# Kernel tuning notes

Hardware: AMD Instinct MI355X
Metric: run time of the kernel (lower is better)

Reference implementation:

```python
import jax, jax.numpy as jnp
import numpy as np

B, N, DE, DH, L, DC = 8, 256, 768, 192, 2, 192
NEG = 1e30  # mask_logic constant from the repo


def setup_inputs() -> dict:
    ks = iter(jax.random.split(jax.random.key(0), 32))

    def nrm(shape, s=0.02):
        return jax.random.normal(next(ks), shape, dtype=jnp.float32) * s

    features = jax.random.normal(next(ks), (B, N, DE), dtype=jnp.float32)
    # DAG adjacency: node i attends to a subset of j < i; guarantee edge (i, i-1)
    rnd = jax.random.bernoulli(next(ks), 0.3, (B, N, N))
    tril = jnp.tril(jnp.ones((N, N), jnp.bool_), -1)
    adj = ((rnd & tril[None]) | jnp.eye(N, k=-1, dtype=jnp.bool_)[None]).astype(jnp.float32)
    s_mask = jax.random.bernoulli(next(ks), 0.5, (B, N, N)).astype(jnp.float32)
    s_mask_onehot = jnp.stack([1.0 - s_mask, s_mask], axis=-1)  # unused in forward
    lengths = jnp.full((B,), N, dtype=jnp.int32)  # unused (nodal_att_type=None)
    return dict(
        features=features, adj=adj, s_mask=s_mask,
        s_mask_onehot=s_mask_onehot, lengths=lengths,
        fc1_w=nrm((DE, DH)), fc1_b=jnp.zeros((DH,), jnp.float32),
        gat_w=nrm((L, 2 * DH)), gat_b=jnp.zeros((L,), jnp.float32),
        wr0=nrm((L, DH, DH)), wr1=nrm((L, DH, DH)),
        gruc_wih=nrm((L, 3 * DH, DH)), gruc_whh=nrm((L, 3 * DH, DH)),
        gruc_bih=jnp.zeros((L, 3 * DH), jnp.float32),
        gruc_bhh=jnp.zeros((L, 3 * DH), jnp.float32),
        grup_wih=nrm((L, 3 * DH, DH)), grup_whh=nrm((L, 3 * DH, DH)),
        grup_bih=jnp.zeros((L, 3 * DH), jnp.float32),
        grup_bhh=jnp.zeros((L, 3 * DH), jnp.float32),
        mlp_w0=nrm((DH * (L + 1), DH)), mlp_b0=jnp.zeros((DH,), jnp.float32),
        mlp_w1=nrm((DH, DH)), mlp_b1=jnp.zeros((DH,), jnp.float32),
        mlp_w2=nrm((DH, DC)), mlp_b2=jnp.zeros((DC,), jnp.float32),
    )


def _gru(x, h, wih, whh, bih, bhh):
    # torch.nn.GRUCell math
    gi = x @ wih.T + bih
    gh = h @ whh.T + bhh
    ir, iz, inn = jnp.split(gi, 3, axis=-1)
    hr, hz, hn = jnp.split(gh, 3, axis=-1)
    r = jax.nn.sigmoid(ir + hr)
    z = jax.nn.sigmoid(iz + hz)
    n = jnp.tanh(inn + r * hn)
    return (1.0 - z) * n + z * h


def _layer(Hl, adj, s_mask, gat_w, gat_b, wr0, wr1, cw, cp):
    # One DAG layer: sequential scan over nodes. Carry holds the relation-
    # projected value buffers V0=H1@Wr0^T, V1=H1@Wr1^T and per-node key
    # scores Ksc=H1@wk (rows >= i are zero and masked out), which is
    # mathematically identical to the torch code that re-projects the
    # growing H1 every step.
    wq, wk = gat_w[:DH], gat_w[DH:]
    pos = jnp.arange(N)

    def step(carry, xs):
        V0, V1, Ksc = carry
        i, x_i, adj_i, sm_i = xs  # x_i:(B,DH) adj_i,sm_i:(B,N)
        score = (x_i @ wq)[:, None] + Ksc + gat_b          # (B,N)
        mask = (pos < i)[None, :] & (adj_i > 0.5)          # ragged :i slice
        alpha = jnp.where(mask, score, score - NEG)        # mask_logic
        attn = jax.nn.softmax(alpha, axis=-1)              # masked -> exactly 0
        Vrel = V0 * sm_i[..., None] + V1 * (1.0 - sm_i[..., None])
        M = jnp.einsum('bn,bnd->bd', attn, Vrel)
        M = jnp.where(i > 0, M, 0.0)                       # node 0: no context
        C = _gru(x_i, M, *cw)
        P = _gru(M, x_i, *cp)
        Hnew = C + P
        V0 = V0.at[:, i, :].set(Hnew @ wr0.T)
        V1 = V1.at[:, i, :].set(Hnew @ wr1.T)
        Ksc = Ksc.at[:, i].set(Hnew @ wk)
        attn_out = jnp.where(i > 0, attn, 0.0)             # adjB row 0 is zeros
        return (V0, V1, Ksc), (Hnew, attn_out)

    z3 = jnp.zeros((B, N, DH), jnp.float32)
    carry0 = (z3, z3, jnp.zeros((B, N), jnp.float32))
    xs = (pos, Hl.transpose(1, 0, 2), adj.transpose(1, 0, 2), s_mask.transpose(1, 0, 2))
    _, (Hseq, Aseq) = jax.lax.scan(step, carry0, xs)
    return Hseq.transpose(1, 0, 2), Aseq.transpose(1, 0, 2)  # (B,N,DH),(B,N,N)


def reference(features, adj, s_mask, s_mask_onehot, lengths,
              fc1_w, fc1_b, gat_w, gat_b, wr0, wr1,
              gruc_wih, gruc_whh, gruc_bih, gruc_bhh,
              grup_wih, grup_whh, grup_bih, grup_bhh,
              mlp_w0, mlp_b0, mlp_w1, mlp_b1, mlp_w2, mlp_b2):
    Hl = jax.nn.relu(features @ fc1_w + fc1_b)  # H0
    Hs, As = [Hl], []
    for l in range(L):
        cw = (gruc_wih[l], gruc_whh[l], gruc_bih[l], gruc_bhh[l])
        cp = (grup_wih[l], grup_whh[l], grup_bih[l], grup_bhh[l])
        Hl, Al = _layer(Hl, adj, s_mask, gat_w[l], gat_b[l], wr0[l], wr1[l], cw, cp)
        Hs.append(Hl)
        As.append(Al)
    H = jnp.concatenate(Hs, axis=2)  # (B,N,DH*(L+1))
    # nodal_att_type=None => attentive_node_features is identity
    h = jax.nn.relu(H @ mlp_w0 + mlp_b0)
    h = jax.nn.relu(h @ mlp_w1 + mlp_b1)  # mlp_layers-1 = 1 extra block
    logits = h @ mlp_w2 + mlp_b2          # dropout: eval-mode identity
    return logits, jnp.stack(As, axis=1)  # (B,N,DC), (B,L,N,N)
```

## Files before the change

### kernel.cpp

```cpp
#include <hip/hip_runtime.h>
#include <stdint.h>

#define B_  8
#define N_  256
#define DH_ 192
#define L_  2
#define G3  576
#define G6  1152
#define NW  4
#define DS  48
#define KD  24
#define GC  288
#define MPSZ (8 * NW * DH_ * 3)
#define KDSZ (8 * NW)
#define STH 10001
#define STP 20001
#define STQ 25001
#define SPK 50000
#define SF1 50001
#define SF2 50002
#define SDN 60001

typedef unsigned long long u64;

__device__ __forceinline__ float bflo(uint32_t u) { return __uint_as_float(u << 16); }
__device__ __forceinline__ float bfhi(uint32_t u) { return __uint_as_float(u & 0xffff0000u); }
__device__ __forceinline__ uint32_t f2bf(float f) {
    uint32_t x = __float_as_uint(f);
    x += 0x7fffu + ((x >> 16) & 1u);
    return x >> 16;
}
__device__ __forceinline__ float sigm(float x)  { return 1.f / (1.f + __expf(-x)); }
__device__ __forceinline__ float tanhf_(float x){ return 1.f - 2.f / (1.f + __expf(2.f * x)); }
__device__ __forceinline__ u64 packvs(float v, int st) {
    return ((u64)(uint32_t)st << 32) | __float_as_uint(v);
}
__device__ __forceinline__ u64 agload(const u64* p) {
    return __hip_atomic_load(p, __ATOMIC_RELAXED, __HIP_MEMORY_SCOPE_AGENT);
}
__device__ __forceinline__ void agstore(u64* p, u64 v) {
    __hip_atomic_store(p, v, __ATOMIC_RELAXED, __HIP_MEMORY_SCOPE_AGENT);
}
__device__ __forceinline__ float u2f(u64 v) { return __uint_as_float((uint32_t)v); }

struct ScanSm {
    uint4 Wr4s[12 * DH_];
    float sA0[2][N_], sA1[2][N_], sKsc[N_];
    float sAdjN[N_], sSmN[N_];
    float sXq[2][DH_];
    float sPre[6 * DS], sXv[DS];
    float sM[DH_], su0[DS], su1[DS], sGc[GC], sHn[DS];
    float sRl[DH_], sP0l[DH_], sP1l[DH_];
    float sRedS[2][8], sRedX[3], sSaved[8], sSavedA[2], sSavedS[2];
};
struct WorkSm {
    float sX[DH_];
    float sPv[GC];
    float sRed[3];
};
struct PrologSm {
    float sA[8][768];
    float sRed[3][8][192];
};
struct MlpSm {
    float sH[8][576];
    float sRed[3][8][192];
    float sT[8][192];
};
union SmemAll { ScanSm s; WorkSm w; PrologSm p; MlpSm m; };

__device__ void prepack_slice(int idx,
    const float* __restrict__ wr0, const float* __restrict__ wr1,
    const float* __restrict__ c_wih, const float* __restrict__ c_whh,
    const float* __restrict__ c_bih, const float* __restrict__ c_bhh,
    const float* __restrict__ p_wih, const float* __restrict__ p_whh,
    const float* __restrict__ p_bih, const float* __restrict__ p_bhh,
    float* __restrict__ WpreT, uint32_t* __restrict__ W4,
    uint32_t* __restrict__ Wr4, uint32_t* __restrict__ Wp4w,
    float* __restrict__ biasPre, float* __restrict__ gbx)
{
    for (int l = 0; l < L_; ++l) {
        const float* cwih = c_wih + l * G3 * DH_;
        const float* cwhh = c_whh + l * G3 * DH_;
        const float* pwih = p_wih + l * G3 * DH_;
        const float* pwhh = p_whh + l * G3 * DH_;
        if (l == 0) {
            int k = idx / G6, r = idx - k * G6;
            float w = (r < G3) ? cwih[r * DH_ + k] : pwhh[(r - G3) * DH_ + k];
            WpreT[k * G6 + r] = w;
        }
        if (idx < NW * 27648) {
// ... 101 lines not shown
                const float* b0 = WpreT + t;
                float a0[8] = {0.f,0.f,0.f,0.f,0.f,0.f,0.f,0.f};
                float a1[8] = {0.f,0.f,0.f,0.f,0.f,0.f,0.f,0.f};
                #pragma unroll 4
                for (int k = 0; k < 192; ++k) {
                    float bva = b0[(size_t)k * G6];
                    float bvb = b0[(size_t)k * G6 + 576];
                    #pragma unroll
                    for (int rr = 0; rr < 8; ++rr) {
                        float av = P->sA[rr][k];
                        a0[rr] += av * bva; a1[rr] += av * bvb;
                    }
                }
                #pragma unroll
                for (int rr = 0; rr < 8; ++rr) {
                    PREg[(size_t)(r0 + rr) * G6 + t]       = a0[rr] + bpa;
                    PREg[(size_t)(r0 + rr) * G6 + 576 + t] = a1[rr] + bpb;
                }
            }
            __syncthreads();
        }
    }
    flag_sync(Fp + 192, wgid, t, SF2);
}

__device__ void mlp_tail(char* smem, int wgid, int t,
    const float* __restrict__ Hcat,
    const float* __restrict__ mw0, const float* __restrict__ mb0,
    const float* __restrict__ mw1, const float* __restrict__ mb1,
    const float* __restrict__ mw2, const float* __restrict__ mb2,
    float* __restrict__ out, u64* __restrict__ Fd)
{
    if (t < 64) {
        while ((uint32_t)(agload(&Fd[t]) >> 32) != (uint32_t)SDN) {}
    }
    __syncthreads();
    __threadfence();
    __syncthreads();
    MlpSm* M = (MlpSm*)smem;
    const int c = t % 192, kg = t / 192;
    for (int tt = wgid; tt < 256; tt += 96) {
        const int r0 = tt * 8;
        for (int q = t; q < 1152; q += 576) {
            int r = q / 144, c4 = q % 144;
            *(float4*)&M->sH[r][4 * c4] = *(const float4*)(Hcat + (size_t)(r0 + r) * G3 + 4 * c4);
        }
        __syncthreads();
        {
            const float* bp = mw0 + (size_t)(kg * 192) * 192 + c;
            float acc[8] = {0.f,0.f,0.f,0.f,0.f,0.f,0.f,0.f};
            #pragma unroll 8
            for (int kk = 0; kk < 192; ++kk) {
                float bv = bp[(size_t)kk * 192];
                #pragma unroll
                for (int rr = 0; rr < 8; ++rr) acc[rr] += M->sH[rr][kg * 192 + kk] * bv;
            }
            #pragma unroll
            for (int rr = 0; rr < 8; ++rr) M->sRed[kg][rr][c] = acc[rr];
        }
        __syncthreads();
        if (t < 192) {
            float bv = mb0[t];
            #pragma unroll
            for (int rr = 0; rr < 8; ++rr)
                M->sT[rr][t] = fmaxf(M->sRed[0][rr][t] + M->sRed[1][rr][t] + M->sRed[2][rr][t] + bv, 0.f);
        }
        __syncthreads();
// ... 19 lines not shown
        __syncthreads();
        {
            const float* bp = mw2 + (size_t)(kg * 64) * 192 + c;
            float acc[8] = {0.f,0.f,0.f,0.f,0.f,0.f,0.f,0.f};
            #pragma unroll 8
            for (int kk = 0; kk < 64; ++kk) {
                float bv = bp[(size_t)kk * 192];
                #pragma unroll
                for (int rr = 0; rr < 8; ++rr) acc[rr] += M->sH[rr][kg * 64 + kk] * bv;
            }
            #pragma unroll
            for (int rr = 0; rr < 8; ++rr) M->sRed[kg][rr][c] = acc[rr];
        }
        __syncthreads();
        if (t < 192) {
            float bv = mb2[t];
            #pragma unroll
            for (int rr = 0; rr < 8; ++rr)
                out[(size_t)(r0 + rr) * 192 + t] =
                    M->sRed[0][rr][t] + M->sRed[1][rr][t] + M->sRed[2][rr][t] + bv;
        }
        __syncthreads();
    }
}

template<int ISL2>
__device__ void scan_body(
    ScanSm* S, int b, int w, int t,
    const float* __restrict__ xin, float* __restrict__ hout,
    const float* __restrict__ PREg, const float* __restrict__ adj,
    const float* __restrict__ smask,
    const uint32_t* __restrict__ W4l, const uint32_t* __restrict__ Wr4l,
    const float* __restrict__ gbxl, const float* __restrict__ gatwl,
    uint32_t* __restrict__ Hw, u64* __restrict__ MPsl, u64* __restrict__ Kdl,
    u64* __restrict__ HcW, const u64* __restrict__ HcR,
    const u64* __restrict__ PREcR, const u64* __restrict__ XQcR,
    float* __restrict__ AsB, int sbase)
{
    const int lane = t & 63, wave = t >> 6;
    const int dg0 = w * DS;
    const float* adjB = adj   + (size_t)b * N_ * N_;
    const float* smB  = smask + (size_t)b * N_ * N_;
    const int fi = b * NW;
    const int cB4 = t >> 1, khB4 = t & 1;

    {
        uint32_t* wr = (uint32_t*)S->Wr4s;
        for (int q = t; q < 9216; q += 576) wr[q] = Wr4l[q];
    }
    uint4 wreg[12];
    {
        const uint4* W4v = (const uint4*)W4l;
        #pragma unroll
        for (int p4 = 0; p4 < 12; ++p4) wreg[p4] = W4v[(12 * khB4 + p4) * GC + cB4];
    }
    float wqx = (!ISL2 && t >= 192 && t < 384) ? gatwl[t - 192] : 0.f;
    float wkv = 0.f, g2b = 0.f, g5b = 0.f;
    if (t < DS) { wkv = gatwl[DH_ + dg0 + t]; g2b = gbxl[dg0 + t]; g5b = gbxl[DH_ + dg0 + t]; }
    if (t < N_) { S->sKsc[t] = 0.f; S->sA0[1][t] = 0.f; S->sA1[1][t] = 0.f; }
    if (t < DS) { S->su0[t] = 0.f; S->su1[t] = 0.f; }
    if (t < 5)  S->sRedS[1][t] = 0.f;
    if (w == 0 && t < N_) AsB[t] = 0.f;

    if (!ISL2) {
        if (t < DS) {
            const float* pre = PREg + (size_t)(b * N_) * G6 + dg0 + t;
            S->sPre[t] = pre[0]; S->sPre[DS + t] = pre[192]; S->sPre[2 * DS + t] = pre[384];
            S->sPre[3 * DS + t] = pre[576]; S->sPre[4 * DS + t] = pre[768]; S->sPre[5 * DS + t] = pre[960];
            S->sXv[t] = xin[(size_t)(b * N_) * G3 + dg0 + t];
        }
        for (int q = t; q < 224; q += 576) {
            if (q < 64)       *(float4*)&S->sAdjN[4 * q] = *(const float4*)(adjB + N_ + 4 * q);
            else if (q < 128) { int q2 = q - 64;  *(float4*)&S->sSmN[4 * q2] = *(const float4*)(smB + N_ + 4 * q2); }
            else if (q < 176) { int q2 = q - 128; *(float4*)&S->sXq[1][4 * q2] = *(const float4*)(xin + (size_t)(b * N_ + 1) * G3 + 4 * q2); }
            else              { int q2 = q - 176; *(float4*)&S->sXq[0][4 * q2] = *(const float4*)(xin + (size_t)(b * N_ + 2) * G3 + 4 * q2); }
        }
    } else {
        for (int q = t; q < 321; q += 576) {
            if (q < 64)       *(float4*)&S->sAdjN[4 * q] = *(const float4*)(adjB + N_ + 4 * q);
            else if (q < 128) { int q2 = q - 64;  *(float4*)&S->sSmN[4 * q2] = *(const float4*)(smB + N_ + 4 * q2); }
            else if (q < 176) {
                int d = q - 128;
                const u64* p = HcR + ((size_t)(b * N_) * NW + w) * DS + d;
                u64 v; do { v = agload(p); } while ((uint32_t)(v >> 32) != (uint32_t)STH);
                S->sXv[d] = __uint_as_float((uint32_t)v);
            } else if (q < 320) {
                int qq = q - 176;
                const u64* p = PREcR + ((size_t)(b * N_) * NW + w) * 144 + qq;
                u64 v; do { v = agload(p); } while ((uint32_t)(v >> 32) != (uint32_t)STP);
                uint32_t pl = (uint32_t)v;
                S->sPre[2 * qq] = bflo(pl); S->sPre[2 * qq + 1] = bfhi(pl);
            } else {
                const u64* p = XQcR + b * N_ + 1;
                u64 v; do { v = agload(p); } while ((uint32_t)(v >> 32) != (uint32_t)(STQ + 1));
                S->sSaved[3] = __uint_as_float((uint32_t)v);
            }
        }
    }
    __syncthreads();
    {
        float hn = 0.f;
        if (t < DS) {
            float xv = S->sXv[t];
            float r1 = sigm(S->sPre[t]), z1 = sigm(S->sPre[DS + t]);
            float n1 = tanhf_(S->sPre[2 * DS + t] + r1 * g2b);
            float Cv = (1.f - z1) * n1;
            float r2 = sigm(S->sPre[3 * DS + t]), z2 = sigm(S->sPre[4 * DS + t]);
            float n2 = tanhf_(g5b + r2 * S->sPre[5 * DS + t]);
            hn = Cv + (1.f - z2) * n2 + z2 * xv;
            S->sHn[t] = hn;
            hout[(size_t)(b * N_) * G3 + dg0 + t] = hn;
            if (!ISL2) HcW[((size_t)(b * N_) * NW + w) * DS + t] = packvs(hn, STH);
        }
        if (t == 0) { S->sSavedA[1] = S->sAdjN[0]; S->sSavedS[1] = S->sSmN[0]; }
        if (wave == 0) {
            float v = hn * wkv;
            #pragma unroll
            for (int o = 32; o; o >>= 1) v += __shfl_xor(v, o);
            if (lane == 0) { S->sSaved[6] = v; agstore(&Kdl[fi + w], packvs(v, sbase)); }
        }
    }
    __syncthreads();
    if (t < KD) Hw[(size_t)t * N_] = f2bf(S->sHn[2 * t]) | (f2bf(S->sHn[2 * t + 1]) << 16);
    if (!ISL2 && t >= 192 && t < 384) {
        float px = S->sXq[1][t - 192] * wqx;
        #pragma unroll
        for (int o = 32; o; o >>= 1) px += __shfl_xor(px, o);
        if (lane == 0) S->sRedX[wave - 3] = px;
    }
    __syncthreads();
    float xqc = ISL2 ? S->sSaved[3] : (S->sRedX[0] + S->sRedX[1] + S->sRedX[2]);

    for (int i = 1; i < N_; ++i) {
        const int row = b * N_ + i;
        const int stamp = sbase + i;
        const int pp = i & 1, pn = pp ^ 1;

        if (t < DH_) {
            float rr = 0.f, p0 = 0.f, p1 = 0.f;
            #pragma unroll 4
            for (int kq = 0; kq < 12; ++kq) {
                uint4 wv = S->Wr4s[kq * DH_ + t];
                const int k0 = 4 * kq;
                float lo, hi;
                lo = bflo(wv.x); hi = bfhi(wv.x);
                rr = fmaf(S->su0[k0 + 0], lo, rr); rr = fmaf(S->su1[k0 + 0], hi, rr);
                p0 = fmaf(S->sHn[k0 + 0], lo, p0); p1 = fmaf(S->sHn[k0 + 0], hi, p1);
                lo = bflo(wv.y); hi = bfhi(wv.y);
                rr = fmaf(S->su0[k0 + 1], lo, rr); rr = fmaf(S->su1[k0 + 1], hi, rr);
                p0 = fmaf(S->sHn[k0 + 1], lo, p0); p1 = fmaf(S->sHn[k0 + 1], hi, p1);
                lo = bflo(wv.z); hi = bfhi(wv.z);
                rr = fmaf(S->su0[k0 + 2], lo, rr); rr = fmaf(S->su1[k0 + 2], hi, rr);
                p0 = fmaf(S->sHn[k0 + 2], lo, p0); p1 = fmaf(S->sHn[k0 + 2], hi, p1);
                lo = bflo(wv.w); hi = bfhi(wv.w);
                rr = fmaf(S->su0[k0 + 3], lo, rr); rr = fmaf(S->su1[k0 + 3], hi, rr);
                p0 = fmaf(S->sHn[k0 + 3], lo, p0); p1 = fmaf(S->sHn[k0 + 3], hi, p1);
            }
            S->sRl[t] = rr; S->sP0l[t] = p0; S->sP1l[t] = p1;
            u64* base = &MPsl[(size_t)pp * MPSZ + ((size_t)(fi + w) * DH_ + t) * 3];
            agstore(base + 0, packvs(rr, stamp));
            agstore(base + 1, packvs(p0, stamp));
            agstore(base + 2, packvs(p1, stamp));
        } else if (t < 384) {
            if (!ISL2) {
                float px = S->sXq[(i - 1) & 1][t - 192] * wqx;
                #pragma unroll
                for (int o = 32; o; o >>= 1) px += __shfl_xor(px, o);
                if (lane == 0) S->sRedX[wave - 3] = px;
            }
        } else {
            const int u = t - 384;
            const int inx = (i + 1 < N_) ? i + 1 : N_ - 1;
            if (!ISL2) {
                const int ixq = (i + 2 < N_) ? i + 2 : N_ - 1;
                for (int qq = u; qq < 260; qq += 192) {
                    if (qq < 64)
                        *(float4*)&S->sAdjN[4 * qq] = *(const float4*)(adjB + (size_t)inx * N_ + 4 * qq);
                    else if (qq < 128) { int q2 = qq - 64;
                        *(float4*)&S->sSmN[4 * q2] = *(const float4*)(smB + (size_t)inx * N_ + 4 * q2); }
                    else if (qq < 140) { int q2 = qq - 128;
                        *(float4*)&S->sXv[4 * q2] = *(const float4*)(xin + (size_t)row * G3 + dg0 + 4 * q2); }
                    else if (qq < 212) { int q2 = qq - 140; int g = q2 / 12, o = q2 - 12 * g;
                        *(float4*)&S->sPre[g * DS + 4 * o] =
                            *(const float4*)(PREg + (size_t)row * G6 + g * DH_ + dg0 + 4 * o); }
                    else { int q2 = qq - 212;
                        *(float4*)&S->sXq[i & 1][4 * q2] = *(const float4*)(xin + (size_t)(b * N_ + ixq) * G3 + 4 * q2); }
                }
            } else {
                for (int qq = u; qq < 321; qq += 192) {
                    if (qq < 64)
                        *(float4*)&S->sAdjN[4 * qq] = *(const float4*)(adjB + (size_t)inx * N_ + 4 * qq);
                    else if (qq < 128) { int q2 = qq - 64;
                        *(float4*)&S->sSmN[4 * q2] = *(const float4*)(smB + (size_t)inx * N_ + 4 * q2); }
                    else if (qq < 176) {
                        int d = qq - 128;
                        const u64* p = HcR + ((size_t)row * NW + w) * DS + d;
                        u64 v; do { v = agload(p); } while ((uint32_t)(v >> 32) != (uint32_t)(STH + i));
                        S->sXv[d] = __uint_as_float((uint32_t)v);
                    } else if (qq < 320) {
                        int q2 = qq - 176;
                        const u64* p = PREcR + ((size_t)row * NW + w) * 144 + q2;
                        u64 v; do { v = agload(p); } while ((uint32_t)(v >> 32) != (uint32_t)(STP + i));
                        uint32_t pl = (uint32_t)v;
                        S->sPre[2 * q2] = bflo(pl); S->sPre[2 * q2 + 1] = bfhi(pl);
                    } else {
                        const u64* p = XQcR + b * N_ + inx;
                        u64 v; do { v = agload(p); } while ((uint32_t)(v >> 32) != (uint32_t)(STQ + inx));
                        S->sSaved[3] = __uint_as_float((uint32_t)v);
                    }
                }
            }
        }
        __syncthreads();

        const float xqn = ISL2 ? S->sSaved[3] : (S->sRedX[0] + S->sRedX[1] + S->sRedX[2]);
        if (t < N_) {
            float e = 0.f;
            if (t == i) { S->sSavedA[pn] = S->sAdjN[t]; S->sSavedS[pn] = S->sSmN[t]; }
            if (t < i - 1 && S->sAdjN[t] > 0.5f) e = __expf(xqn + S->sKsc[t]);
            float b0 = e * S->sSmN[t];
            S->sA0[pn][t] = b0; S->sA1[pn][t] = e - b0;
            float ps = e;
            #pragma unroll
            for (int o = 32; o; o >>= 1) ps += __shfl_xor(ps, o);
            if (lane == 0) S->sRedS[pn][wave] = ps;
        }
        __syncthreads();

        if (t < 384) {
            const int ilim = i - 1;
            const int kd = t >> 4, jp = t & 15;
            const uint32_t* hp = Hw + (size_t)kd * N_;
            float u0l = 0.f, u0h = 0.f, u1l = 0.f, u1h = 0.f;
            int j = jp;
            while (j + 48 < ilim) {
                uint32_t h0 = hp[j], h1 = hp[j + 16], h2 = hp[j + 32], h3 = hp[j + 48];
                float b0, b1;
                b0 = S->sA0[pn][j];      b1 = S->sA1[pn][j];
                u0l = fmaf(b0, bflo(h0), u0l); u0h = fmaf(b0, bfhi(h0), u0h);
                u1l = fmaf(b1, bflo(h0), u1l); u1h = fmaf(b1, bfhi(h0), u1h);
                b0 = S->sA0[pn][j + 16]; b1 = S->sA1[pn][j + 16];
                u0l = fmaf(b0, bflo(h1), u0l); u0h = fmaf(b0, bfhi(h1), u0h);
                u1l = fmaf(b1, bflo(h1), u1l); u1h = fmaf(b1, bfhi(h1), u1h);
                b0 = S->sA0[pn][j + 32]; b1 = S->sA1[pn][j + 32];
                u0l = fmaf(b0, bflo(h2), u0l); u0h = fmaf(b0, bfhi(h2), u0h);
                u1l = fmaf(b1, bflo(h2), u1l); u1h = fmaf(b1, bfhi(h2), u1h);
                b0 = S->sA0[pn][j + 48]; b1 = S->sA1[pn][j + 48];
                u0l = fmaf(b0, bflo(h3), u0l); u0h = fmaf(b0, bfhi(h3), u0h);
                u1l = fmaf(b1, bflo(h3), u1l); u1h = fmaf(b1, bfhi(h3), u1h);
                j += 64;
            }
            for (; j < ilim; j += 16) {
                uint32_t hv = hp[j];
                float b0 = S->sA0[pn][j], b1 = S->sA1[pn][j];
                u0l = fmaf(b0, bflo(hv), u0l); u0h = fmaf(b0, bfhi(hv), u0h);
                u1l = fmaf(b1, bflo(hv), u1l); u1h = fmaf(b1, bfhi(hv), u1h);
            }
            #pragma unroll
            for (int o = 1; o <= 8; o <<= 1) {
                u0l += __shfl_xor(u0l, o); u0h += __shfl_xor(u0h, o);
                u1l += __shfl_xor(u1l, o); u1h += __shfl_xor(u1h, o);
            }
            if (jp == 0) {
                S->su0[2 * kd] = u0l; S->su0[2 * kd + 1] = u0h;
                S->su1[2 * kd] = u1l; S->su1[2 * kd + 1] = u1h;
            }
        } else {
            const int d = t - 384;
            const int w1 = (w + 1) & 3, w2 = (w + 2) & 3, w3 = (w + 3) & 3;
            const u64* pA = &MPsl[(size_t)pp * MPSZ + ((size_t)(fi + w1) * DH_ + d) * 3];
            const u64* pB = &MPsl[(size_t)pp * MPSZ + ((size_t)(fi + w2) * DH_ + d) * 3];
            const u64* pC = &MPsl[(size_t)pp * MPSZ + ((size_t)(fi + w3) * DH_ + d) * 3];
            const uint32_t ex = (uint32_t)stamp;
            u64 a0, a1, a2, b0, b1, b2, c0, c1, c2;
            do {
                a0 = agload(pA); a1 = agload(pA + 1); a2 = agload(pA + 2);
                b0 = agload(pB); b1 = agload(pB + 1); b2 = agload(pB + 2);
                c0 = agload(pC); c1 = agload(pC + 1); c2 = agload(pC + 2);
            } while ((uint32_t)(a0 >> 32) != ex || (uint32_t)(a1 >> 32) != ex ||
                     (uint32_t)(a2 >> 32) != ex || (uint32_t)(b0 >> 32) != ex ||
                     (uint32_t)(b1 >> 32) != ex || (uint32_t)(b2 >> 32) != ex ||
                     (uint32_t)(c0 >> 32) != ex || (uint32_t)(c1 >> 32) != ex ||
                     (uint32_t)(c2 >> 32) != ex);
            S->sRl[d]  += u2f(a0) + u2f(b0) + u2f(c0);
            S->sP0l[d] += u2f(a1) + u2f(b1) + u2f(c1);
            S->sP1l[d] += u2f(a2) + u2f(b2) + u2f(c2);
            if (t == 575) {
                const uint32_t ex2 = (uint32_t)(stamp - 1);
                const int kpar = (i - 1) & 1;
                u64 k0, k1, k2;
                u64* q1 = &Kdl[kpar * KDSZ + fi + w1];
                u64* q2 = &Kdl[kpar * KDSZ + fi + w2];
                u64* q3 = &Kdl[kpar * KDSZ + fi + w3];
                do {
                    k0 = agload(q1); k1 = agload(q2); k2 = agload(q3);
                } while ((uint32_t)(k0 >> 32) != ex2 || (uint32_t)(k1 >> 32) != ex2 ||
                         (uint32_t)(k2 >> 32) != ex2);
                float kdot = S->sSaved[6] + u2f(k0) + u2f(k1) + u2f(k2);
                float adj1 = S->sSavedA[pp], sm1 = S->sSavedS[pp];
                float e1 = (adj1 > 0.5f) ? __expf(xqc + kdot) : 0.f;
                float Ssum = S->sRedS[pp][0] + S->sRedS[pp][1] + S->sRedS[pp][2]
                           + S->sRedS[pp][3] + S->sRedS[pp][4] + e1;
                S->sKsc[i - 1] = kdot;
                float invS = 1.f / Ssum;
                float e1c0 = e1 * sm1, e1c1 = e1 - e1c0;
                S->sSaved[2] = invS;
                S->sSaved[4] = e1c0; S->sSaved[5] = e1c1;
                S->sA0[pp][i - 1] = e1c0; S->sA1[pp][i - 1] = e1c1;
                float adjn = S->sAdjN[i - 1], smn = S->sSmN[i - 1];
                float en = (adjn > 0.5f) ? __expf(xqn + kdot) : 0.f;
                float n0 = en * smn;
                S->sA0[pn][i - 1] = n0; S->sA1[pn][i - 1] = en - n0;
                S->sRedS[pn][4] = en;
            }
        }
        __syncthreads();

        if (t < DH_) {
            S->sM[t] = (S->sRl[t] + S->sSaved[4] * S->sP0l[t]
                                  + S->sSaved[5] * S->sP1l[t]) * S->sSaved[2];
        } else if (t < 192 + DS) {
            const int k = t - 192;
            float a0 = S->sA0[pn][i - 1], a1 = S->sA1[pn][i - 1];
            S->su0[k] += a0 * S->sHn[k];
            S->su1[k] += a1 * S->sHn[k];
        } else if (w == 0 && t >= 256 && t < 512) {
            const int j = t - 256;
            AsB[(size_t)i * N_ + j] = (S->sA0[pp][j] + S->sA1[pp][j]) * S->sSaved[2];
        }
        __syncthreads();

        {
            float g = 0.f;
            #pragma unroll
            for (int p4 = 0; p4 < 12; ++p4) {
                const uint4 wv = wreg[p4];
                const int m0 = 8 * (12 * khB4 + p4);
                g = fmaf(S->sM[m0 + 0], bflo(wv.x), g); g = fmaf(S->sM[m0 + 1], bfhi(wv.x), g);
                g = fmaf(S->sM[m0 + 2], bflo(wv.y), g); g = fmaf(S->sM[m0 + 3], bfhi(wv.y), g);
                g = fmaf(S->sM[m0 + 4], bflo(wv.z), g); g = fmaf(S->sM[m0 + 5], bfhi(wv.z), g);
                g = fmaf(S->sM[m0 + 6], bflo(wv.w), g); g = fmaf(S->sM[m0 + 7], bfhi(wv.w), g);
            }
            g += __shfl_xor(g, 1);
            if (khB4 == 0) S->sGc[cB4] = g;
        }
        __syncthreads();

        {
            float hn = 0.f;
            if (t < DS) {
                float Mv = S->sM[dg0 + t];
                float r1 = sigm(S->sPre[t] + S->sGc[t]);
                float z1 = sigm(S->sPre[DS + t] + S->sGc[DS + t]);
                float n1 = tanhf_(S->sPre[2 * DS + t] + r1 * (S->sGc[2 * DS + t] + g2b));
                float Cv = (1.f - z1) * n1 + z1 * Mv;
                float r2 = sigm(S->sGc[3 * DS + t] + S->sPre[3 * DS + t]);
                float z2 = sigm(S->sGc[4 * DS + t] + S->sPre[4 * DS + t]);
                float n2 = tanhf_(S->sGc[5 * DS + t] + g5b + r2 * S->sPre[5 * DS + t]);
                hn = Cv + (1.f - z2) * n2 + z2 * S->sXv[t];
                S->sHn[t] = hn;
                hout[(size_t)row * G3 + dg0 + t] = hn;
                if (!ISL2) HcW[((size_t)row * NW + w) * DS + t] = packvs(hn, STH + i);
            }
            if (wave == 0) {
                float v = hn * wkv;
                #pragma unroll
                for (int o = 32; o; o >>= 1) v += __shfl_xor(v, o);
                if (lane == 0) { S->sSaved[6] = v; agstore(&Kdl[pp * KDSZ + fi + w], packvs(v, stamp)); }
            }
            if (t < KD) Hw[(size_t)t * N_ + i] = f2bf(S->sHn[2 * t]) | (f2bf(S->sHn[2 * t + 1]) << 16);
        }
        __syncthreads();
        xqc = xqn;
    }
}

__device__ void worker_body(WorkSm* Wm, int b, int w, int t,
    const uint32_t* __restrict__ Wp4g, const float* __restrict__ bias2,
    const float* __restrict__ wq2,
    const u64* __restrict__ HcR, u64* __restrict__ PREcW, u64* __restrict__ XQcW)
{
    const int lane = t & 63, wave = t >> 6;
    const int c = t >> 1, kh = t & 1;
    uint4 wpreg[12];
    {
        const uint4* v4 = (const uint4*)Wp4g;
        #pragma unroll
        for (int p4 = 0; p4 < 12; ++p4) wpreg[p4] = v4[(12 * kh + p4) * GC + c];
    }
    float bv = 0.f;
    if (kh == 0) bv = bias2[192 * (c / DS) + w * DS + (c % DS)];
    float wqt = (t < DH_) ? wq2[t] : 0.f;
    for (int i = 0; i < N_; ++i) {
        if (t < DH_) {
            const u64* p = HcR + ((size_t)(b * N_ + i) * NW + (t / DS)) * DS + (t % DS);
            u64 v; do { v = agload(p); } while ((uint32_t)(v >> 32) != (uint32_t)(STH + i));
            Wm->sX[t] = __uint_as_float((uint32_t)v);
        }
        __syncthreads();
        {
            float g = 0.f;
            #pragma unroll
            for (int p4 = 0; p4 < 12; ++p4) {
                const uint4 wv = wpreg[p4];
                const int m0 = 8 * (12 * kh + p4);
                g = fmaf(Wm->sX[m0 + 0], bflo(wv.x), g); g = fmaf(Wm->sX[m0 + 1], bfhi(wv.x), g);
                g = fmaf(Wm->sX[m0 + 2], bflo(wv.y), g); g = fmaf(Wm->sX[m0 + 3], bfhi(wv.y), g);
                g = fmaf(Wm->sX[m0 + 4], bflo(wv.z), g); g = fmaf(Wm->sX[m0 + 5], bfhi(wv.z), g);
                g = fmaf(Wm->sX[m0 + 6], bflo(wv.w), g); g = fmaf(Wm->sX[m0 + 7], bfhi(wv.w), g);
            }
            g += __shfl_xor(g, 1);
            if (kh == 0) Wm->sPv[c] = g + bv;
        }
        if (w == 0) {
            float px = (t < DH_) ? Wm->sX[t] * wqt : 0.f;
            #pragma unroll
            for (int o = 32; o; o >>= 1) px += __shfl_xor(px, o);
            if (t < DH_ && lane == 0) Wm->sRed[wave] = px;
        }
        __syncthreads();
        if (t < 144) {
            u64 v = ((u64)(uint32_t)(STP + i) << 32)
                  | f2bf(Wm->sPv[2 * t]) | (f2bf(Wm->sPv[2 * t + 1]) << 16);
            agstore(&PREcW[((size_t)(b * N_ + i) * NW + w) * 144 + t], v);
        }
        if (w == 0 && t == 0)
            agstore(&XQcW[b * N_ + i],
                    packvs(Wm->sRed[0] + Wm->sRed[1] + Wm->sRed[2], STQ + i));
        __syncthreads();
    }
}

__global__ __launch_bounds__(576, 1) void pipeline_kernel(
    const float* __restrict__ features, const float* __restrict__ fc1_w,
    const float* __restrict__ fc1_b,
    const float* __restrict__ adj, const float* __restrict__ smask,
    const float* __restrict__ gatw,
    const float* __restrict__ wr0, const float* __restrict__ wr1,
    const float* __restrict__ c_wih, const float* __restrict__ c_whh,
    const float* __restrict__ c_bih, const float* __restrict__ c_bhh,
    const float* __restrict__ p_wih, const float* __restrict__ p_whh,
    const float* __restrict__ p_bih, const float* __restrict__ p_bhh,
    const float* __restrict__ mw0, const float* __restrict__ mb0,
    const float* __restrict__ mw1, const float* __restrict__ mb1,
    const float* __restrict__ mw2, const float* __restrict__ mb2,
    float* __restrict__ Hcat, float* __restrict__ PREg,
    float* __restrict__ WpreT, uint32_t* __restrict__ W4,
    uint32_t* __restrict__ Wr4, uint32_t* __restrict__ Wp4w,
    float* __restrict__ biasPre, float* __restrict__ gbx,
    uint32_t* __restrict__ Hb, u64* __restrict__ MPs, u64* __restrict__ Kd,
    u64* __restrict__ Hc, u64* __restrict__ PREc, u64* __restrict__ XQc,
    u64* __restrict__ Fp, u64* __restrict__ Fd,
    float* __restrict__ out)
{
    __shared__ __align__(16) char smem[sizeof(SmemAll)];
    const int blk = blockIdx.x, t = threadIdx.x;
    const int wgid = blk;
    const int b = blk & 7, r12 = blk >> 3;
    const int role = r12 >> 2, w = r12 & 3;

    for (int j = 0; j < 4; ++j) {
        int idx = wgid * 576 + t + 55296 * j;
        prepack_slice(idx, wr0, wr1, c_wih, c_whh, c_bih, c_bhh,
                      p_wih, p_whh, p_bih, p_bhh,
                      WpreT, W4, Wr4, Wp4w, biasPre, gbx);
    }
    flag_sync(Fp, wgid, t, SPK);

    prologue(smem, wgid, t, features, fc1_w, fc1_b, WpreT, biasPre,
             Hcat, PREg, Fp);

    float* As = out + 393216;
    if (role == 0) {
        scan_body<0>((ScanSm*)smem, b, w, t,
            Hcat, Hcat + 192, PREg, adj, smask,
            W4, Wr4, gbx, gatw,
            Hb + (size_t)(b * NW + w) * KD * N_, MPs, Kd,
            Hc, nullptr, nullptr, nullptr,
            As + (size_t)b * (L_ * N_ * N_), 1);
        __threadfence();
        __syncthreads();
        if (t == 0) agstore(&Fd[b * 8 + w], packvs(0.f, SDN));
    } else if (role == 2) {
        scan_body<1>((ScanSm*)smem, b, w, t,
            nullptr, Hcat + 384, nullptr, adj, smask,
            W4 + NW * 27648, Wr4 + NW * 9216, gbx + 384, gatw + 384,
            Hb + (size_t)(32 + b * NW + w) * KD * N_,
            MPs + (size_t)2 * MPSZ, Kd + 2 * KDSZ,
            nullptr, Hc, PREc, XQc,
            As + (size_t)b * (L_ * N_ * N_) + N_ * N_, 30001);
        __threadfence();
        __syncthreads();
        if (t == 0) agstore(&Fd[b * 8 + 4 + w], packvs(0.f, SDN));
    } else {
        worker_body((WorkSm*)smem, b, w, t,
            Wp4w + (size_t)w * 27648, biasPre + G6, gatw + 384,
            Hc, PREc, XQc);
    }

    mlp_tail(smem, wgid, t, Hcat, mw0, mb0, mw1, mb1, mw2, mb2, out, Fd);
}

extern "C" void kernel_launch(void* const* d_in, const int* in_sizes, int n_in,
                              void* d_out, int out_size, void* d_ws, size_t ws_size,
                              hipStream_t stream)
{
    const float* features = (const float*)d_in[0];
    const float* adj      = (const float*)d_in[1];
    const float* smask    = (const float*)d_in[2];
    const float* fc1_w = (const float*)d_in[5];
    const float* fc1_b = (const float*)d_in[6];
    const float* gat_w = (const float*)d_in[7];
    const float* wr0   = (const float*)d_in[9];
    const float* wr1   = (const float*)d_in[10];
    const float* c_wih = (const float*)d_in[11];
    const float* c_whh = (const float*)d_in[12];
    const float* c_bih = (const float*)d_in[13];
    const float* c_bhh = (const float*)d_in[14];
    const float* p_wih = (const float*)d_in[15];
    const float* p_whh = (const float*)d_in[16];
    const float* p_bih = (const float*)d_in[17];
    const float* p_bhh = (const float*)d_in[18];
    const float* mw0 = (const float*)d_in[19];
    const float* mb0 = (const float*)d_in[20];
    const float* mw1 = (const float*)d_in[21];
    const float* mb1 = (const float*)d_in[22];
    const float* mw2 = (const float*)d_in[23];
    const float* mb2 = (const float*)d_in[24];
    float* out = (float*)d_out;

    char* wsb = (char*)d_ws;
    size_t off = 0;
    auto carve = [&](size_t bytes) -> char* {
        char* p = wsb + off;
        off = (off + bytes + 255) & ~(size_t)255;
        return p;
    };
    float* Hcat     = (float*)carve(2048ull * 576 * 4);
    float* PREg     = (float*)carve(2048ull * 1152 * 4);
    float* WpreT    = (float*)carve(192ull * 1152 * 4);
    uint32_t* W4    = (uint32_t*)carve(2ull * NW * 27648 * 4);
    uint32_t* Wr4   = (uint32_t*)carve(2ull * NW * 9216 * 4);
    uint32_t* Wp4w  = (uint32_t*)carve((size_t)NW * 27648 * 4);
    float* biasPre  = (float*)carve(2ull * 1152 * 4);
    float* gbx      = (float*)carve(2ull * 384 * 4);
    uint32_t* Hb    = (uint32_t*)carve(64ull * KD * 256 * 4);
    u64* MPs        = (u64*)carve(4ull * MPSZ * 8);
    u64* Kd         = (u64*)carve(4ull * KDSZ * 8);
    u64* Hc         = (u64*)carve(8ull * 256 * NW * DS * 8);
    u64* PREc       = (u64*)carve(8ull * 256 * NW * 144 * 8);
    u64* XQc        = (u64*)carve(8ull * 256 * 8);
    u64* Fp         = (u64*)carve(288ull * 8);
    u64* Fd         = (u64*)carve(64ull * 8);

    pipeline_kernel<<<dim3(96), 576, 0, stream>>>(
        features, fc1_w, fc1_b, adj, smask, gat_w,
        wr0, wr1, c_wih, c_whh, c_bih, c_bhh, p_wih, p_whh, p_bih, p_bhh,
        mw0, mb0, mw1, mb1, mw2, mb2,
        Hcat, PREg, WpreT, W4, Wr4, Wp4w, biasPre, gbx,
        Hb, MPs, Kd, Hc, PREc, XQc, Fp, Fd, out);
}
```

Measured before the change: 1.737 ms.

## Use per-workgroup ready flags for message exchange and drop softmax query term

Partial message sums (r, p0, p1) and key dots are now written as plain floats. Each workgroup publishes a single stamped flag per step after a threadfence, replacing the earlier scheme that stamped every element with a 64-bit tag and spun on all nine values. The query-projection term xq is removed from the attention exponent, since it is constant across a row and cancels in the softmax normalisation. That removes its per-step reductions, the cross-block XQ channel and the worker reductions. Spin loops gain s_sleep backoff. The risk is memory-ordering mistakes with relaxed flag/data stores and larger raw exp arguments without the shift.

```diff
diff --git a/kernel.cpp b/kernel.cpp
--- a/kernel.cpp
+++ b/kernel.cpp
@@ -11,11 +11,11 @@
 #define DS  48
 #define KD  24
 #define GC  288
-#define MPSZ (8 * NW * DH_ * 3)
-#define KDSZ (8 * NW)
+#define MSGR (2 * 8 * NW * 576)
+#define KDR  (2 * 8 * NW)
+#define MFR  (2 * 8 * NW)
 #define STH 10001
 #define STP 20001
-#define STQ 25001
 #define SPK 50000
 #define SF1 50001
 #define SF2 50002
@@ -41,22 +41,23 @@
 __device__ __forceinline__ void agstore(u64* p, u64 v) {
     __hip_atomic_store(p, v, __ATOMIC_RELAXED, __HIP_MEMORY_SCOPE_AGENT);
 }
+__device__ __forceinline__ float agloadf(const float* p) {
+    return __hip_atomic_load(p, __ATOMIC_RELAXED, __HIP_MEMORY_SCOPE_AGENT);
+}
 __device__ __forceinline__ float u2f(u64 v) { return __uint_as_float((uint32_t)v); }
 
 struct ScanSm {
     uint4 Wr4s[12 * DH_];
     float sA0[2][N_], sA1[2][N_], sKsc[N_];
     float sAdjN[N_], sSmN[N_];
-    float sXq[2][DH_];
     float sPre[6 * DS], sXv[DS];
     float sM[DH_], su0[DS], su1[DS], sGc[GC], sHn[DS];
     float sRl[DH_], sP0l[DH_], sP1l[DH_];
-    float sRedS[2][8], sRedX[3], sSaved[8], sSavedA[2], sSavedS[2];
+    float sRedS[2][8], sSaved[8], sSavedA[2], sSavedS[2];
 };
 struct WorkSm {
     float sX[DH_];
     float sPv[GC];
-    float sRed[3];
 };
 struct PrologSm {
     float sA[8][768];
@@ -224,7 +225,8 @@
     float* __restrict__ out, u64* __restrict__ Fd)
 {
     if (t < 64) {
-        while ((uint32_t)(agload(&Fd[t]) >> 32) != (uint32_t)SDN) {}
+        while ((uint32_t)(agload(&Fd[t]) >> 32) != (uint32_t)SDN)
+            __builtin_amdgcn_s_sleep(2);
     }
     __syncthreads();
     __threadfence();
@@ -310,9 +312,10 @@
     const float* __restrict__ smask,
     const uint32_t* __restrict__ W4l, const uint32_t* __restrict__ Wr4l,
     const float* __restrict__ gbxl, const float* __restrict__ gatwl,
-    uint32_t* __restrict__ Hw, u64* __restrict__ MPsl, u64* __restrict__ Kdl,
+    uint32_t* __restrict__ Hw,
+    float* __restrict__ MSGl, float* __restrict__ KdAl, u64* __restrict__ MFl,
     u64* __restrict__ HcW, const u64* __restrict__ HcR,
-    const u64* __restrict__ PREcR, const u64* __restrict__ XQcR,
+    const u64* __restrict__ PREcR,
     float* __restrict__ AsB, int sbase)
 {
     const int lane = t & 63, wave = t >> 6;
@@ -321,6 +324,7 @@
     const float* smB  = smask + (size_t)b * N_ * N_;
     const int fi = b * NW;
     const int cB4 = t >> 1, khB4 = t & 1;
+    const int w1 = (w + 1) & 3, w2 = (w + 2) & 3, w3 = (w + 3) & 3;
 
     {
         uint32_t* wr = (uint32_t*)S->Wr4s;
@@ -332,12 +336,11 @@
         #pragma unroll
         for (int p4 = 0; p4 < 12; ++p4) wreg[p4] = W4v[(12 * khB4 + p4) * GC + cB4];
     }
-    float wqx = (!ISL2 && t >= 192 && t < 384) ? gatwl[t - 192] : 0.f;
     float wkv = 0.f, g2b = 0.f, g5b = 0.f;
     if (t < DS) { wkv = gatwl[DH_ + dg0 + t]; g2b = gbxl[dg0 + t]; g5b = gbxl[DH_ + dg0 + t]; }
     if (t < N_) { S->sKsc[t] = 0.f; S->sA0[1][t] = 0.f; S->sA1[1][t] = 0.f; }
     if (t < DS) { S->su0[t] = 0.f; S->su1[t] = 0.f; }
-    if (t < 5)  S->sRedS[1][t] = 0.f;
+    if (t < 8)  S->sRedS[1][t] = 0.f;
     if (w == 0 && t < N_) AsB[t] = 0.f;
 
     if (!ISL2) {
@@ -347,14 +350,12 @@
             S->sPre[3 * DS + t] = pre[576]; S->sPre[4 * DS + t] = pre[768]; S->sPre[5 * DS + t] = pre[960];
             S->sXv[t] = xin[(size_t)(b * N_) * G3 + dg0 + t];
         }
-        for (int q = t; q < 224; q += 576) {
-            if (q < 64)       *(float4*)&S->sAdjN[4 * q] = *(const float4*)(adjB + N_ + 4 * q);
-            else if (q < 128) { int q2 = q - 64;  *(float4*)&S->sSmN[4 * q2] = *(const float4*)(smB + N_ + 4 * q2); }
-            else if (q < 176) { int q2 = q - 128; *(float4*)&S->sXq[1][4 * q2] = *(const float4*)(xin + (size_t)(b * N_ + 1) * G3 + 4 * q2); }
-            else              { int q2 = q - 176; *(float4*)&S->sXq[0][4 * q2] = *(const float4*)(xin + (size_t)(b * N_ + 2) * G3 + 4 * q2); }
+        for (int q = t; q < 128; q += 576) {
+            if (q < 64)  *(float4*)&S->sAdjN[4 * q] = *(const float4*)(adjB + N_ + 4 * q);
+            else { int q2 = q - 64; *(float4*)&S->sSmN[4 * q2] = *(const float4*)(smB + N_ + 4 * q2); }
         }
     } else {
-        for (int q = t; q < 321; q += 576) {
+        for (int q = t; q < 320; q += 576) {
             if (q < 64)       *(float4*)&S->sAdjN[4 * q] = *(const float4*)(adjB + N_ + 4 * q);
             else if (q < 128) { int q2 = q - 64;  *(float4*)&S->sSmN[4 * q2] = *(const float4*)(smB + N_ + 4 * q2); }
             else if (q < 176) {
@@ -362,16 +363,12 @@
                 const u64* p = HcR + ((size_t)(b * N_) * NW + w) * DS + d;
                 u64 v; do { v = agload(p); } while ((uint32_t)(v >> 32) != (uint32_t)STH);
                 S->sXv[d] = __uint_as_float((uint32_t)v);
-            } else if (q < 320) {
+            } else {
                 int qq = q - 176;
                 const u64* p = PREcR + ((size_t)(b * N_) * NW + w) * 144 + qq;
                 u64 v; do { v = agload(p); } while ((uint32_t)(v >> 32) != (uint32_t)STP);
                 uint32_t pl = (uint32_t)v;
                 S->sPre[2 * qq] = bflo(pl); S->sPre[2 * qq + 1] = bfhi(pl);
-            } else {
-                const u64* p = XQcR + b * N_ + 1;
-                u64 v; do { v = agload(p); } while ((uint32_t)(v >> 32) != (uint32_t)(STQ + 1));
-                S->sSaved[3] = __uint_as_float((uint32_t)v);
             }
         }
     }
@@ -395,19 +392,12 @@
             float v = hn * wkv;
             #pragma unroll
             for (int o = 32; o; o >>= 1) v += __shfl_xor(v, o);
-            if (lane == 0) { S->sSaved[6] = v; agstore(&Kdl[fi + w], packvs(v, sbase)); }
+            if (lane == 0) { S->sSaved[6] = v; KdAl[fi + w] = v; }
         }
     }
     __syncthreads();
     if (t < KD) Hw[(size_t)t * N_] = f2bf(S->sHn[2 * t]) | (f2bf(S->sHn[2 * t + 1]) << 16);
-    if (!ISL2 && t >= 192 && t < 384) {
-        float px = S->sXq[1][t - 192] * wqx;
-        #pragma unroll
-        for (int o = 32; o; o >>= 1) px += __shfl_xor(px, o);
-        if (lane == 0) S->sRedX[wave - 3] = px;
-    }
     __syncthreads();
-    float xqc = ISL2 ? S->sSaved[3] : (S->sRedX[0] + S->sRedX[1] + S->sRedX[2]);
 
     for (int i = 1; i < N_; ++i) {
         const int row = b * N_ + i;
@@ -435,37 +425,26 @@
                 p0 = fmaf(S->sHn[k0 + 3], lo, p0); p1 = fmaf(S->sHn[k0 + 3], hi, p1);
             }
             S->sRl[t] = rr; S->sP0l[t] = p0; S->sP1l[t] = p1;
-            u64* base = &MPsl[(size_t)pp * MPSZ + ((size_t)(fi + w) * DH_ + t) * 3];
-            agstore(base + 0, packvs(rr, stamp));
-            agstore(base + 1, packvs(p0, stamp));
-            agstore(base + 2, packvs(p1, stamp));
-        } else if (t < 384) {
-            if (!ISL2) {
-                float px = S->sXq[(i - 1) & 1][t - 192] * wqx;
-                #pragma unroll
-                for (int o = 32; o; o >>= 1) px += __shfl_xor(px, o);
-                if (lane == 0) S->sRedX[wave - 3] = px;
-            }
-        } else {
+            float* myMSG = MSGl + (size_t)(pp * 32 + fi + w) * 576;
+            myMSG[t] = rr; myMSG[192 + t] = p0; myMSG[384 + t] = p1;
+            __threadfence();
+        } else if (t >= 384) {
             const int u = t - 384;
             const int inx = (i + 1 < N_) ? i + 1 : N_ - 1;
             if (!ISL2) {
-                const int ixq = (i + 2 < N_) ? i + 2 : N_ - 1;
-                for (int qq = u; qq < 260; qq += 192) {
+                for (int qq = u; qq < 212; qq += 192) {
                     if (qq < 64)
                         *(float4*)&S->sAdjN[4 * qq] = *(const float4*)(adjB + (size_t)inx * N_ + 4 * qq);
                     else if (qq < 128) { int q2 = qq - 64;
                         *(float4*)&S->sSmN[4 * q2] = *(const float4*)(smB + (size_t)inx * N_ + 4 * q2); }
                     else if (qq < 140) { int q2 = qq - 128;
                         *(float4*)&S->sXv[4 * q2] = *(const float4*)(xin + (size_t)row * G3 + dg0 + 4 * q2); }
-                    else if (qq < 212) { int q2 = qq - 140; int g = q2 / 12, o = q2 - 12 * g;
+                    else { int q2 = qq - 140; int g = q2 / 12, o = q2 - 12 * g;
                         *(float4*)&S->sPre[g * DS + 4 * o] =
                             *(const float4*)(PREg + (size_t)row * G6 + g * DH_ + dg0 + 4 * o); }
-                    else { int q2 = qq - 212;
-                        *(float4*)&S->sXq[i & 1][4 * q2] = *(const float4*)(xin + (size_t)(b * N_ + ixq) * G3 + 4 * q2); }
                 }
             } else {
-                for (int qq = u; qq < 321; qq += 192) {
+                for (int qq = u; qq < 320; qq += 192) {
                     if (qq < 64)
                         *(float4*)&S->sAdjN[4 * qq] = *(const float4*)(adjB + (size_t)inx * N_ + 4 * qq);
                     else if (qq < 128) { int q2 = qq - 64;
@@ -475,27 +454,23 @@
                         const u64* p = HcR + ((size_t)row * NW + w) * DS + d;
                         u64 v; do { v = agload(p); } while ((uint32_t)(v >> 32) != (uint32_t)(STH + i));
                         S->sXv[d] = __uint_as_float((uint32_t)v);
-                    } else if (qq < 320) {
+                    } else {
                         int q2 = qq - 176;
                         const u64* p = PREcR + ((size_t)row * NW + w) * 144 + q2;
                         u64 v; do { v = agload(p); } while ((uint32_t)(v >> 32) != (uint32_t)(STP + i));
                         uint32_t pl = (uint32_t)v;
                         S->sPre[2 * q2] = bflo(pl); S->sPre[2 * q2 + 1] = bfhi(pl);
-                    } else {
-                        const u64* p = XQcR + b * N_ + inx;
-                        u64 v; do { v = agload(p); } while ((uint32_t)(v >> 32) != (uint32_t)(STQ + inx));
-                        S->sSaved[3] = __uint_as_float((uint32_t)v);
                     }
                 }
             }
         }
         __syncthreads();
 
-        const float xqn = ISL2 ? S->sSaved[3] : (S->sRedX[0] + S->sRedX[1] + S->sRedX[2]);
+        if (t == 0) agstore(&MFl[pp * 32 + fi + w], packvs(0.f, stamp));
         if (t < N_) {
             float e = 0.f;
             if (t == i) { S->sSavedA[pn] = S->sAdjN[t]; S->sSavedS[pn] = S->sSmN[t]; }
-            if (t < i - 1 && S->sAdjN[t] > 0.5f) e = __expf(xqn + S->sKsc[t]);
+            if (t < i - 1 && S->sAdjN[t] > 0.5f) e = __expf(S->sKsc[t]);
             float b0 = e * S->sSmN[t];
             S->sA0[pn][t] = b0; S->sA1[pn][t] = e - b0;
             float ps = e;
@@ -543,60 +518,49 @@
                 S->su0[2 * kd] = u0l; S->su0[2 * kd + 1] = u0h;
                 S->su1[2 * kd] = u1l; S->su1[2 * kd + 1] = u1h;
             }
-        } else {
-            const int d = t - 384;
-            const int w1 = (w + 1) & 3, w2 = (w + 2) & 3, w3 = (w + 3) & 3;
-            const u64* pA = &MPsl[(size_t)pp * MPSZ + ((size_t)(fi + w1) * DH_ + d) * 3];
-            const u64* pB = &MPsl[(size_t)pp * MPSZ + ((size_t)(fi + w2) * DH_ + d) * 3];
-            const u64* pC = &MPsl[(size_t)pp * MPSZ + ((size_t)(fi + w3) * DH_ + d) * 3];
+        } else if (t == 575) {
             const uint32_t ex = (uint32_t)stamp;
-            u64 a0, a1, a2, b0, b1, b2, c0, c1, c2;
-            do {
-                a0 = agload(pA); a1 = agload(pA + 1); a2 = agload(pA + 2);
-                b0 = agload(pB); b1 = agload(pB + 1); b2 = agload(pB + 2);
-                c0 = agload(pC); c1 = agload(pC + 1); c2 = agload(pC + 2);
-            } while ((uint32_t)(a0 >> 32) != ex || (uint32_t)(a1 >> 32) != ex ||
-                     (uint32_t)(a2 >> 32) != ex || (uint32_t)(b0 >> 32) != ex ||
-                     (uint32_t)(b1 >> 32) != ex || (uint32_t)(b2 >> 32) != ex ||
-                     (uint32_t)(c0 >> 32) != ex || (uint32_t)(c1 >> 32) != ex ||
-                     (uint32_t)(c2 >> 32) != ex);
-            S->sRl[d]  += u2f(a0) + u2f(b0) + u2f(c0);
-            S->sP0l[d] += u2f(a1) + u2f(b1) + u2f(c1);
-            S->sP1l[d] += u2f(a2) + u2f(b2) + u2f(c2);
-            if (t == 575) {
-                const uint32_t ex2 = (uint32_t)(stamp - 1);
-                const int kpar = (i - 1) & 1;
-                u64 k0, k1, k2;
-                u64* q1 = &Kdl[kpar * KDSZ + fi + w1];
-                u64* q2 = &Kdl[kpar * KDSZ + fi + w2];
-                u64* q3 = &Kdl[kpar * KDSZ + fi + w3];
-                do {
-                    k0 = agload(q1); k1 = agload(q2); k2 = agload(q3);
-                } while ((uint32_t)(k0 >> 32) != ex2 || (uint32_t)(k1 >> 32) != ex2 ||
-                         (uint32_t)(k2 >> 32) != ex2);
-                float kdot = S->sSaved[6] + u2f(k0) + u2f(k1) + u2f(k2);
-                float adj1 = S->sSavedA[pp], sm1 = S->sSavedS[pp];
-                float e1 = (adj1 > 0.5f) ? __expf(xqc + kdot) : 0.f;
-                float Ssum = S->sRedS[pp][0] + S->sRedS[pp][1] + S->sRedS[pp][2]
-                           + S->sRedS[pp][3] + S->sRedS[pp][4] + e1;
-                S->sKsc[i - 1] = kdot;
-                float invS = 1.f / Ssum;
-                float e1c0 = e1 * sm1, e1c1 = e1 - e1c0;
-                S->sSaved[2] = invS;
-                S->sSaved[4] = e1c0; S->sSaved[5] = e1c1;
-                S->sA0[pp][i - 1] = e1c0; S->sA1[pp][i - 1] = e1c1;
-                float adjn = S->sAdjN[i - 1], smn = S->sSmN[i - 1];
-                float en = (adjn > 0.5f) ? __expf(xqn + kdot) : 0.f;
-                float n0 = en * smn;
-                S->sA0[pn][i - 1] = n0; S->sA1[pn][i - 1] = en - n0;
-                S->sRedS[pn][4] = en;
-            }
+            const u64* f1 = &MFl[pp * 32 + fi + w1];
+            const u64* f2 = &MFl[pp * 32 + fi + w2];
+            const u64* f3 = &MFl[pp * 32 + fi + w3];
+            for (;;) {
+                u64 a = agload(f1), bq = agload(f2), c = agload(f3);
+                if ((uint32_t)(a >> 32) == ex && (uint32_t)(bq >> 32) == ex &&
+                    (uint32_t)(c >> 32) == ex) break;
+                __builtin_amdgcn_s_sleep(1);
+            }
+            const int kpar = (i - 1) & 1;
+            float kdot = S->sSaved[6]
+                       + agloadf(&KdAl[kpar * 32 + fi + w1])
+                       + agloadf(&KdAl[kpar * 32 + fi + w2])
+                       + agloadf(&KdAl[kpar * 32 + fi + w3]);
+            float adj1 = S->sSavedA[pp], sm1 = S->sSavedS[pp];
+            float er = __expf(kdot);
+            float e1 = (adj1 > 0.5f) ? er : 0.f;
+            float Ssum = S->sRedS[pp][0] + S->sRedS[pp][1] + S->sRedS[pp][2]
+                       + S->sRedS[pp][3] + S->sRedS[pp][4] + e1;
+            S->sKsc[i - 1] = kdot;
+            float invS = 1.f / Ssum;
+            float e1c0 = e1 * sm1, e1c1 = e1 - e1c0;
+            S->sSaved[2] = invS;
+            S->sSaved[4] = e1c0; S->sSaved[5] = e1c1;
+            S->sA0[pp][i - 1] = e1c0; S->sA1[pp][i - 1] = e1c1;
+            float adjn = S->sAdjN[i - 1], smn = S->sSmN[i - 1];
+            float en = (adjn > 0.5f) ? er : 0.f;
+            float n0 = en * smn;
+            S->sA0[pn][i - 1] = n0; S->sA1[pn][i - 1] = en - n0;
+            S->sRedS[pn][4] = en;
         }
         __syncthreads();
 
         if (t < DH_) {
-            S->sM[t] = (S->sRl[t] + S->sSaved[4] * S->sP0l[t]
-                                  + S->sSaved[5] * S->sP1l[t]) * S->sSaved[2];
+            const float* m1 = MSGl + (size_t)(pp * 32 + fi + w1) * 576;
+            const float* m2 = MSGl + (size_t)(pp * 32 + fi + w2) * 576;
+            const float* m3 = MSGl + (size_t)(pp * 32 + fi + w3) * 576;
+            float rs = S->sRl[t]  + agloadf(m1 + t)       + agloadf(m2 + t)       + agloadf(m3 + t);
+            float p0 = S->sP0l[t] + agloadf(m1 + 192 + t) + agloadf(m2 + 192 + t) + agloadf(m3 + 192 + t);
+            float p1 = S->sP1l[t] + agloadf(m1 + 384 + t) + agloadf(m2 + 384 + t) + agloadf(m3 + 384 + t);
+            S->sM[t] = (rs + S->sSaved[4] * p0 + S->sSaved[5] * p1) * S->sSaved[2];
         } else if (t < 192 + DS) {
             const int k = t - 192;
             float a0 = S->sA0[pn][i - 1], a1 = S->sA1[pn][i - 1];
@@ -644,21 +608,18 @@
                 float v = hn * wkv;
                 #pragma unroll
                 for (int o = 32; o; o >>= 1) v += __shfl_xor(v, o);
-                if (lane == 0) { S->sSaved[6] = v; agstore(&Kdl[pp * KDSZ + fi + w], packvs(v, stamp)); }
+                if (lane == 0) { S->sSaved[6] = v; KdAl[(i & 1) * 32 + fi + w] = v; }
             }
             if (t < KD) Hw[(size_t)t * N_ + i] = f2bf(S->sHn[2 * t]) | (f2bf(S->sHn[2 * t + 1]) << 16);
         }
         __syncthreads();
-        xqc = xqn;
     }
 }
 
 __device__ void worker_body(WorkSm* Wm, int b, int w, int t,
     const uint32_t* __restrict__ Wp4g, const float* __restrict__ bias2,
-    const float* __restrict__ wq2,
-    const u64* __restrict__ HcR, u64* __restrict__ PREcW, u64* __restrict__ XQcW)
+    const u64* __restrict__ HcR, u64* __restrict__ PREcW)
 {
-    const int lane = t & 63, wave = t >> 6;
     const int c = t >> 1, kh = t & 1;
     uint4 wpreg[12];
     {
@@ -668,7 +629,6 @@
     }
     float bv = 0.f;
     if (kh == 0) bv = bias2[192 * (c / DS) + w * DS + (c % DS)];
-    float wqt = (t < DH_) ? wq2[t] : 0.f;
     for (int i = 0; i < N_; ++i) {
         if (t < DH_) {
             const u64* p = HcR + ((size_t)(b * N_ + i) * NW + (t / DS)) * DS + (t % DS);
@@ -690,21 +650,12 @@
             g += __shfl_xor(g, 1);
             if (kh == 0) Wm->sPv[c] = g + bv;
         }
-        if (w == 0) {
-            float px = (t < DH_) ? Wm->sX[t] * wqt : 0.f;
-            #pragma unroll
-            for (int o = 32; o; o >>= 1) px += __shfl_xor(px, o);
-            if (t < DH_ && lane == 0) Wm->sRed[wave] = px;
-        }
         __syncthreads();
         if (t < 144) {
             u64 v = ((u64)(uint32_t)(STP + i) << 32)
                   | f2bf(Wm->sPv[2 * t]) | (f2bf(Wm->sPv[2 * t + 1]) << 16);
             agstore(&PREcW[((size_t)(b * N_ + i) * NW + w) * 144 + t], v);
         }
-        if (w == 0 && t == 0)
-            agstore(&XQcW[b * N_ + i],
-                    packvs(Wm->sRed[0] + Wm->sRed[1] + Wm->sRed[2], STQ + i));
         __syncthreads();
     }
 }
@@ -726,8 +677,9 @@
     float* __restrict__ WpreT, uint32_t* __restrict__ W4,
     uint32_t* __restrict__ Wr4, uint32_t* __restrict__ Wp4w,
     float* __restrict__ biasPre, float* __restrict__ gbx,
-    uint32_t* __restrict__ Hb, u64* __restrict__ MPs, u64* __restrict__ Kd,
-    u64* __restrict__ Hc, u64* __restrict__ PREc, u64* __restrict__ XQc,
+    uint32_t* __restrict__ Hb,
+    float* __restrict__ MSG, float* __restrict__ KdA, u64* __restrict__ MFlag,
+    u64* __restrict__ Hc, u64* __restrict__ PREc,
     u64* __restrict__ Fp, u64* __restrict__ Fd,
     float* __restrict__ out)
 {
@@ -753,8 +705,9 @@
         scan_body<0>((ScanSm*)smem, b, w, t,
             Hcat, Hcat + 192, PREg, adj, smask,
             W4, Wr4, gbx, gatw,
-            Hb + (size_t)(b * NW + w) * KD * N_, MPs, Kd,
-            Hc, nullptr, nullptr, nullptr,
+            Hb + (size_t)(b * NW + w) * KD * N_,
+            MSG, KdA, MFlag,
+            Hc, nullptr, nullptr,
             As + (size_t)b * (L_ * N_ * N_), 1);
         __threadfence();
         __syncthreads();
@@ -764,16 +717,16 @@
             nullptr, Hcat + 384, nullptr, adj, smask,
             W4 + NW * 27648, Wr4 + NW * 9216, gbx + 384, gatw + 384,
             Hb + (size_t)(32 + b * NW + w) * KD * N_,
-            MPs + (size_t)2 * MPSZ, Kd + 2 * KDSZ,
-            nullptr, Hc, PREc, XQc,
+            MSG + MSGR, KdA + KDR, MFlag + MFR,
+            nullptr, Hc, PREc,
             As + (size_t)b * (L_ * N_ * N_) + N_ * N_, 30001);
         __threadfence();
         __syncthreads();
         if (t == 0) agstore(&Fd[b * 8 + 4 + w], packvs(0.f, SDN));
     } else {
         worker_body((WorkSm*)smem, b, w, t,
-            Wp4w + (size_t)w * 27648, biasPre + G6, gatw + 384,
-            Hc, PREc, XQc);
+            Wp4w + (size_t)w * 27648, biasPre + G6,
+            Hc, PREc);
     }
 
     mlp_tail(smem, wgid, t, Hcat, mw0, mb0, mw1, mb1, mw2, mb2, out, Fd);
@@ -823,11 +776,11 @@
     float* biasPre  = (float*)carve(2ull * 1152 * 4);
     float* gbx      = (float*)carve(2ull * 384 * 4);
     uint32_t* Hb    = (uint32_t*)carve(64ull * KD * 256 * 4);
-    u64* MPs        = (u64*)carve(4ull * MPSZ * 8);
-    u64* Kd         = (u64*)carve(4ull * KDSZ * 8);
+    float* MSG      = (float*)carve(2ull * MSGR * 4);
+    float* KdA      = (float*)carve(2ull * KDR * 4);
+    u64* MFlag      = (u64*)carve(2ull * MFR * 8);
     u64* Hc         = (u64*)carve(8ull * 256 * NW * DS * 8);
     u64* PREc       = (u64*)carve(8ull * 256 * NW * 144 * 8);
-    u64* XQc        = (u64*)carve(8ull * 256 * 8);
     u64* Fp         = (u64*)carve(288ull * 8);
     u64* Fd         = (u64*)carve(64ull * 8);
 
@@ -836,5 +789,5 @@
         wr0, wr1, c_wih, c_whh, c_bih, c_bhh, p_wih, p_whh, p_bih, p_bhh,
         mw0, mb0, mw1, mb1, mw2, mb2,
         Hcat, PREg, WpreT, W4, Wr4, Wp4w, biasPre, gbx,
-        Hb, MPs, Kd, Hc, PREc, XQc, Fp, Fd, out);
-}
+        Hb, MSG, KdA, MFlag, Hc, PREc, Fp, Fd, out);
+}
```

After: 2.364 ms. +36.1%, slower.
